# Performance work log

Hardware: AMD Instinct MI355X
Metric: run time of the kernel (lower is better)

The kernel has to match this reference:

```python
import jax, jax.numpy as jnp
import numpy as np

# Model dims (match init_kwargs)
U, I, E = 100000, 50000, 1000000   # users, items, interactions
FD, EK, EF = 64, 64, 64            # feature_dim, embed_k, embed_f
L = 3                              # n_layers
B = 16384                          # scoring batch
ALPHA = [1.0 / (k + 1) for k in range(L + 1)]


def setup_inputs() -> dict:
    key = jax.random.key(0)
    ks = jax.random.split(key, 9)
    Gu = jax.random.normal(ks[0], (U, EK), jnp.float32) * 0.05
    Gi = jax.random.normal(ks[1], (I, EK), jnp.float32) * 0.05
    F = jax.random.normal(ks[2], (FD, EF), jnp.float32) * 0.1
    proj_w = jax.random.normal(ks[3], (EF, 1), jnp.float32) * 0.1
    proj_b = jnp.zeros((1,), jnp.float32)
    # sparse binary-ish decomposition-path feature matrix (dense here)
    edge_features = (jax.random.uniform(ks[4], (E, FD)) < 0.1).astype(jnp.float32)
    u = jax.random.randint(ks[5], (E,), 0, U)
    it = jax.random.randint(ks[6], (E,), 0, I) + U  # items offset by num_users
    edge_index = jnp.stack([jnp.concatenate([u, it]),
                            jnp.concatenate([it, u])]).astype(jnp.int64)  # [2, 2E]
    users = jax.random.randint(ks[7], (B,), 0, U).astype(jnp.int64)
    items = jax.random.randint(ks[8], (B,), 0, I).astype(jnp.int64)
    return dict(Gu=Gu, Gi=Gi, F=F, proj_w=proj_w, proj_b=proj_b,
                edge_features=edge_features, edge_index=edge_index,
                users=users, items=items)


def _propagate(Gu, Gi, F, proj_w, proj_b, edge_features, edge_index):
    N = U + I
    src, dst = edge_index[0], edge_index[1]
    # edge-feature projection -> scalar edge weight, duplicated per direction
    ew = (edge_features @ F) @ proj_w + proj_b            # [E, 1]
    ew = jnp.concatenate([ew, ew], axis=0)[:, 0]          # [2E]
    # symmetric GCN normalization over the bipartite interaction graph
    deg = jax.ops.segment_sum(jnp.ones_like(ew), dst, num_segments=N)  # [N]
    dinv = jnp.where(deg > 0, jax.lax.rsqrt(jnp.maximum(deg, 1.0)), 0.0)
    coef = (dinv[src] * dinv[dst] * ew)[:, None]          # [2E, 1]
    x = jnp.concatenate([Gu, Gi], axis=0)                 # [N, K]
    out = ALPHA[0] * x
    for k in range(L):  # edge-conditioned gather -> scale -> scatter-add
        x = jax.ops.segment_sum(coef * x[src], dst, num_segments=N)
        out = out + ALPHA[k + 1] * x
    return out[:U], out[U:]


def reference(Gu, Gi, F, proj_w, proj_b, edge_features, edge_index, users, items):
    gu, gi = _propagate(Gu, Gi, F, proj_w, proj_b, edge_features, edge_index)
    # forward(): masked dot-product scoring of (user, item) pairs
    return jnp.sum(gu[users] * gi[items], axis=1)  # [B]
```

## Files before the change

### kernel.cpp

```cpp
#include <hip/hip_runtime.h>

constexpr int Uc = 100000;
constexpr int Ic = 50000;
constexpr int Nc = 150000;
constexpr int Ec = 1000000;
constexpr int Bc = 16384;
constexpr int NBS = (Nc + 1023) / 1024;

typedef _Float16 h16;
union H8 { uint4 u; h16 h[8]; };


__global__ void k_zero(uint4* __restrict__ deg4) {
    int i = blockIdx.x * blockDim.x + threadIdx.x;
    if (i < Nc / 4) deg4[i] = make_uint4(0u, 0u, 0u, 0u);
}

__global__ void k_deg2_fproj(const int* __restrict__ un, const int* __restrict__ in_,
                             unsigned* __restrict__ deg,
                             const float* __restrict__ F, const float* __restrict__ pw,
                             float* __restrict__ Fp) {
    if (blockIdx.x == 0 && threadIdx.x < 64) {
        int d = threadIdx.x;
        float s = 0.f;
#pragma unroll
        for (int j = 0; j < 64; ++j) s += F[d * 64 + j] * pw[j];
        Fp[d] = s;
    }
    int e = blockIdx.x * blockDim.x + threadIdx.x;
    if (e < Ec) {
        atomicAdd(&deg[un[e]], 1u);
        atomicAdd(&deg[in_[e]], 1u);
    }
}

__global__ void k_scan1(const unsigned* __restrict__ deg, int* __restrict__ rowptr,
                        int* __restrict__ bsums, float* __restrict__ dinv) {
    __shared__ int sh[256];
    int tid = threadIdx.x, bid = blockIdx.x;
    int base = bid * 1024 + tid * 4;
    int v0 = (base + 0 < Nc) ? (int)deg[base + 0] : 0;
    int v1 = (base + 1 < Nc) ? (int)deg[base + 1] : 0;
    int v2 = (base + 2 < Nc) ? (int)deg[base + 2] : 0;
    int v3 = (base + 3 < Nc) ? (int)deg[base + 3] : 0;
    if (base + 0 < Nc) dinv[base + 0] = v0 ? rsqrtf((float)v0) : 0.f;
    if (base + 1 < Nc) dinv[base + 1] = v1 ? rsqrtf((float)v1) : 0.f;
    if (base + 2 < Nc) dinv[base + 2] = v2 ? rsqrtf((float)v2) : 0.f;
    if (base + 3 < Nc) dinv[base + 3] = v3 ? rsqrtf((float)v3) : 0.f;
    int s = v0 + v1 + v2 + v3;
    sh[tid] = s;
    __syncthreads();
    for (int off = 1; off < 256; off <<= 1) {
        int t = (tid >= off) ? sh[tid - off] : 0;
        __syncthreads();
        sh[tid] += t;
        __syncthreads();
    }
    int excl = sh[tid] - s;
    if (tid == 255) bsums[bid] = sh[255];
    if (base + 0 < Nc) rowptr[base + 0] = excl;
    if (base + 1 < Nc) rowptr[base + 1] = excl + v0;
    if (base + 2 < Nc) rowptr[base + 2] = excl + v0 + v1;
    if (base + 3 < Nc) rowptr[base + 3] = excl + v0 + v1 + v2;
}

__global__ void k_scan3(int* __restrict__ rowptr, const int* __restrict__ bsums,
                        int* __restrict__ cursor) {
    __shared__ int sh[256];
    int tid = threadIdx.x;
    int v = (tid < NBS) ? bsums[tid] : 0;
    sh[tid] = v;
    __syncthreads();
    for (int off = 1; off < 256; off <<= 1) {
        int t = (tid >= off) ? sh[tid - off] : 0;
        __syncthreads();
        sh[tid] += t;
        __syncthreads();
    }
    int excl = sh[tid] - v;
    __syncthreads();
    sh[tid] = excl;
    __syncthreads();
    int i = blockIdx.x * blockDim.x + threadIdx.x;
    if (i < Nc) {
        int r = rowptr[i] + sh[i >> 10];
        rowptr[i] = r;
        cursor[i] = r;
    }
    if (i == 0) rowptr[Nc] = 2 * Ec;
}

__global__ void k_build(const int* __restrict__ un, const int* __restrict__ in_,
                        const float* __restrict__ ef, const float* __restrict__ Fp,
                        const float* __restrict__ pb, const float* __restrict__ dinv,
                        int* __restrict__ cursor, int2* __restrict__ csr) {
    int t = blockIdx.x * blockDim.x + threadIdx.x;
    int e = t >> 4, l = t & 15;
    if (e >= Ec) return;
    float4 f = reinterpret_cast<const float4*>(ef)[(size_t)e * 16 + l];
    float4 w = reinterpret_cast<const float4*>(Fp)[l];
    float s = f.x * w.x + f.y * w.y + f.z * w.z + f.w * w.w;
    s += __shfl_xor(s, 8, 16);
    s += __shfl_xor(s, 4, 16);
    s += __shfl_xor(s, 2, 16);
    s += __shfl_xor(s, 1, 16);
    if (l == 0 || l == 8) {
        int uu = un[e], ii = in_[e];
        float c = dinv[uu] * dinv[ii] * (s + pb[0]);
        if (l == 0) {
            int pos = atomicAdd(&cursor[ii], 1);
            csr[pos] = make_int2(uu, __float_as_int(c));
        } else {
            int pos = atomicAdd(&cursor[uu], 1);
            csr[pos] = make_int2(ii, __float_as_int(c));
        }
    }
}

__global__ void k_xin(const float* __restrict__ Gu, const float* __restrict__ Gi,
                      uint4* __restrict__ xin) {
    int t = blockIdx.x * blockDim.x + threadIdx.x;
    if (t >= Nc * 8) return;
    const float4* g;
    int idx;
    if (t < Uc * 8) { g = reinterpret_cast<const float4*>(Gu); idx = t * 2; }
    else            { g = reinterpret_cast<const float4*>(Gi); idx = (t - Uc * 8) * 2; }
    float4 a = g[idx], b = g[idx + 1];
    H8 o;
    o.h[0] = (h16)a.x; o.h[1] = (h16)a.y; o.h[2] = (h16)a.z; o.h[3] = (h16)a.w;
    o.h[4] = (h16)b.x; o.h[5] = (h16)b.y; o.h[6] = (h16)b.z; o.h[7] = (h16)b.w;
    xin[t] = o.u;
}

__global__ void k_gprop(const int* __restrict__ rowptr, const int2* __restrict__ csr,
                        const uint4* __restrict__ x, uint4* __restrict__ xn,
                        int n0, int n1) {
    int t = blockIdx.x * blockDim.x + threadIdx.x;
    int n = n0 + (t >> 3), l = t & 7;
    if (n >= n1) return;
    int e0 = rowptr[n], e1 = rowptr[n + 1];
    float acc[8] = {0.f, 0.f, 0.f, 0.f, 0.f, 0.f, 0.f, 0.f};
    int e = e0;
    for (; e + 4 <= e1; e += 4) {
        int2 s0 = csr[e], s1 = csr[e + 1], s2 = csr[e + 2], s3 = csr[e + 3];
        H8 v0, v1, v2, v3;
        v0.u = x[s0.x * 8 + l];
        v1.u = x[s1.x * 8 + l];
        v2.u = x[s2.x * 8 + l];
        v3.u = x[s3.x * 8 + l];
        float c0 = __int_as_float(s0.y), c1 = __int_as_float(s1.y);
        float c2 = __int_as_float(s2.y), c3 = __int_as_float(s3.y);
#pragma unroll
        for (int j = 0; j < 8; ++j)
            acc[j] += c0 * (float)v0.h[j] + c1 * (float)v1.h[j]
                    + c2 * (float)v2.h[j] + c3 * (float)v3.h[j];
    }
    for (; e < e1; ++e) {
        int2 sc = csr[e];
        float c = __int_as_float(sc.y);
        H8 v; v.u = x[sc.x * 8 + l];
#pragma unroll
        for (int j = 0; j < 8; ++j) acc[j] += c * (float)v.h[j];
    }
    H8 o;
#pragma unroll
    for (int j = 0; j < 8; ++j) o.h[j] = (h16)acc[j];
    xn[n * 8 + l] = o.u;
}

__global__ void k_final(const float* __restrict__ Gu, const float* __restrict__ Gi,
                        const uint4* __restrict__ x1, const uint4* __restrict__ x2,
                        const int* __restrict__ rowptr, const int2* __restrict__ csr,
                        const int* __restrict__ users, const int* __restrict__ items,
                        float* __restrict__ out) {
    int t = blockIdx.x * blockDim.x + threadIdx.x;
    int wid = t >> 3, j8 = t & 7;
    if (wid >= Bc) return;
    int un = users[wid];
    int in_ = Uc + items[wid];

    float a2[2][8];
#pragma unroll
    for (int side = 0; side < 2; ++side) {
        int n = side ? in_ : un;
        const float4* g = side ? reinterpret_cast<const float4*>(Gi)
                               : reinterpret_cast<const float4*>(Gu);
        int gi = (side ? (n - Uc) : n) * 16 + 2 * j8;
        float4 ba = g[gi], bb = g[gi + 1];
        H8 h1, h2;
        h1.u = x1[(size_t)n * 8 + j8];
        h2.u = x2[(size_t)n * 8 + j8];
        float a[8];
        a[0] = ba.x; a[1] = ba.y; a[2] = ba.z; a[3] = ba.w;
        a[4] = bb.x; a[5] = bb.y; a[6] = bb.z; a[7] = bb.w;
#pragma unroll
        for (int j = 0; j < 8; ++j)
            a[j] += 0.5f * (float)h1.h[j] + (1.f / 3.f) * (float)h2.h[j];

        float su[8] = {0.f, 0.f, 0.f, 0.f, 0.f, 0.f, 0.f, 0.f};
        int e0 = rowptr[n], e1 = rowptr[n + 1];
        int e = e0;
        for (; e + 4 <= e1; e += 4) {
            int2 s0 = csr[e], s1 = csr[e + 1], s2 = csr[e + 2], s3 = csr[e + 3];
            H8 v0, v1, v2, v3;
            v0.u = x2[(size_t)s0.x * 8 + j8];
            v1.u = x2[(size_t)s1.x * 8 + j8];
            v2.u = x2[(size_t)s2.x * 8 + j8];
            v3.u = x2[(size_t)s3.x * 8 + j8];
            float c0 = __int_as_float(s0.y), c1 = __int_as_float(s1.y);
            float c2 = __int_as_float(s2.y), c3 = __int_as_float(s3.y);
#pragma unroll
            for (int j = 0; j < 8; ++j)
                su[j] += c0 * (float)v0.h[j] + c1 * (float)v1.h[j]
                       + c2 * (float)v2.h[j] + c3 * (float)v3.h[j];
        }
        for (; e < e1; ++e) {
            int2 sc = csr[e];
            float c = __int_as_float(sc.y);
            H8 v; v.u = x2[(size_t)sc.x * 8 + j8];
#pragma unroll
            for (int j = 0; j < 8; ++j) su[j] += c * (float)v.h[j];
        }
#pragma unroll
        for (int j = 0; j < 8; ++j) a2[side][j] = a[j] + 0.25f * su[j];
    }

    float p = 0.f;
#pragma unroll
    for (int j = 0; j < 8; ++j) p += a2[0][j] * a2[1][j];
    p += __shfl_xor(p, 4, 8);
    p += __shfl_xor(p, 2, 8);
    p += __shfl_xor(p, 1, 8);
    if (j8 == 0) out[wid] = p;
}


extern "C" void kernel_launch(void* const* d_in, const int* in_sizes, int n_in,
                              void* d_out, int out_size, void* d_ws, size_t ws_size,
                              hipStream_t stream) {
    const float* Gu = (const float*)d_in[0];
    const float* Gi = (const float*)d_in[1];
    const float* F  = (const float*)d_in[2];
    const float* pw = (const float*)d_in[3];
    const float* pb = (const float*)d_in[4];
    const float* ef = (const float*)d_in[5];
    const int*   ei = (const int*)d_in[6];
    const int* users = (const int*)d_in[7];
    const int* items = (const int*)d_in[8];
    float* out = (float*)d_out;

    float* ws = (float*)d_ws;
    float*    Fp     = ws;
    float*    dinv   = Fp + 64;
    unsigned* deg    = (unsigned*)(dinv + Nc);
    int*      rowptr = (int*)(deg + Nc);
    int*      cursor = rowptr + (Nc + 16);
    int*      bsums  = cursor + Nc;
    int2*     csr    = (int2*)(bsums + 256);
    h16*      xin    = (h16*)(csr + 2 * Ec);
    h16*      xa     = xin + (size_t)Nc * 64;
    h16*      xb     = xa + (size_t)Nc * 64;

    const int* un  = ei;
    const int* in_ = ei + 2 * Ec;

    k_zero<<<(Nc / 4 + 255) / 256, 256, 0, stream>>>((uint4*)deg);
    k_deg2_fproj<<<(Ec + 255) / 256, 256, 0, stream>>>(un, in_, deg, F, pw, Fp);
    k_scan1<<<NBS, 256, 0, stream>>>(deg, rowptr, bsums, dinv);
    k_scan3<<<(Nc + 255) / 256, 256, 0, stream>>>(rowptr, bsums, cursor);
    k_build<<<(Ec * 16) / 256, 256, 0, stream>>>(un, in_, ef, Fp, pb, dinv, cursor, csr);
    k_xin<<<(Nc * 8 + 255) / 256, 256, 0, stream>>>(Gu, Gi, (uint4*)xin);

    k_gprop<<<(Uc * 8 + 255) / 256, 256, 0, stream>>>(rowptr, csr, (const uint4*)xin, (uint4*)xa, 0, Uc);
    k_gprop<<<((Nc - Uc) * 8 + 255) / 256, 256, 0, stream>>>(rowptr, csr, (const uint4*)xin, (uint4*)xa, Uc, Nc);
    k_gprop<<<(Uc * 8 + 255) / 256, 256, 0, stream>>>(rowptr, csr, (const uint4*)xa, (uint4*)xb, 0, Uc);
    k_gprop<<<((Nc - Uc) * 8 + 255) / 256, 256, 0, stream>>>(rowptr, csr, (const uint4*)xa, (uint4*)xb, Uc, Nc);

    k_final<<<(Bc * 8 + 255) / 256, 256, 0, stream>>>(Gu, Gi, (const uint4*)xa, (const uint4*)xb,
                                                      rowptr, csr, users, items, out);
}
```

Baseline: 360.0 us.

## Fuse all stages into one cooperative persistent kernel with grid syncs

Replaces the chain of separate launches (zeroing, degree count, scans, CSR build, fp16 conversion, two propagation passes, final scoring) with a single cooperative kernel. Grid-stride loops cover each stage and grid.sync() separates them. The aim is to remove per-launch overhead and inter-kernel gaps. In exchange, occupancy is capped by the persistent grid size, and each grid-wide barrier has its own cost. The user and item propagation halves are also merged into one pass.

```diff
diff --git a/kernel.cpp b/kernel.cpp
--- a/kernel.cpp
+++ b/kernel.cpp
@@ -1,4 +1,7 @@
 #include <hip/hip_runtime.h>
+#include <hip/hip_cooperative_groups.h>
+
+namespace cg = cooperative_groups;
 
 constexpr int Uc = 100000;
 constexpr int Ic = 50000;
@@ -10,272 +13,281 @@
 typedef _Float16 h16;
 union H8 { uint4 u; h16 h[8]; };
 
-
-__global__ void k_zero(uint4* __restrict__ deg4) {
-    int i = blockIdx.x * blockDim.x + threadIdx.x;
-    if (i < Nc / 4) deg4[i] = make_uint4(0u, 0u, 0u, 0u);
-}
-
-__global__ void k_deg2_fproj(const int* __restrict__ un, const int* __restrict__ in_,
-                             unsigned* __restrict__ deg,
-                             const float* __restrict__ F, const float* __restrict__ pw,
-                             float* __restrict__ Fp) {
-    if (blockIdx.x == 0 && threadIdx.x < 64) {
-        int d = threadIdx.x;
-        float s = 0.f;
-#pragma unroll
-        for (int j = 0; j < 64; ++j) s += F[d * 64 + j] * pw[j];
-        Fp[d] = s;
-    }
-    int e = blockIdx.x * blockDim.x + threadIdx.x;
-    if (e < Ec) {
-        atomicAdd(&deg[un[e]], 1u);
-        atomicAdd(&deg[in_[e]], 1u);
-    }
-}
-
-__global__ void k_scan1(const unsigned* __restrict__ deg, int* __restrict__ rowptr,
-                        int* __restrict__ bsums, float* __restrict__ dinv) {
-    __shared__ int sh[256];
-    int tid = threadIdx.x, bid = blockIdx.x;
-    int base = bid * 1024 + tid * 4;
-    int v0 = (base + 0 < Nc) ? (int)deg[base + 0] : 0;
-    int v1 = (base + 1 < Nc) ? (int)deg[base + 1] : 0;
-    int v2 = (base + 2 < Nc) ? (int)deg[base + 2] : 0;
-    int v3 = (base + 3 < Nc) ? (int)deg[base + 3] : 0;
-    if (base + 0 < Nc) dinv[base + 0] = v0 ? rsqrtf((float)v0) : 0.f;
-    if (base + 1 < Nc) dinv[base + 1] = v1 ? rsqrtf((float)v1) : 0.f;
-    if (base + 2 < Nc) dinv[base + 2] = v2 ? rsqrtf((float)v2) : 0.f;
-    if (base + 3 < Nc) dinv[base + 3] = v3 ? rsqrtf((float)v3) : 0.f;
-    int s = v0 + v1 + v2 + v3;
-    sh[tid] = s;
-    __syncthreads();
-    for (int off = 1; off < 256; off <<= 1) {
-        int t = (tid >= off) ? sh[tid - off] : 0;
-        __syncthreads();
-        sh[tid] += t;
-        __syncthreads();
-    }
-    int excl = sh[tid] - s;
-    if (tid == 255) bsums[bid] = sh[255];
-    if (base + 0 < Nc) rowptr[base + 0] = excl;
-    if (base + 1 < Nc) rowptr[base + 1] = excl + v0;
-    if (base + 2 < Nc) rowptr[base + 2] = excl + v0 + v1;
-    if (base + 3 < Nc) rowptr[base + 3] = excl + v0 + v1 + v2;
-}
-
-__global__ void k_scan3(int* __restrict__ rowptr, const int* __restrict__ bsums,
-                        int* __restrict__ cursor) {
-    __shared__ int sh[256];
-    int tid = threadIdx.x;
-    int v = (tid < NBS) ? bsums[tid] : 0;
-    sh[tid] = v;
-    __syncthreads();
-    for (int off = 1; off < 256; off <<= 1) {
-        int t = (tid >= off) ? sh[tid - off] : 0;
-        __syncthreads();
-        sh[tid] += t;
-        __syncthreads();
-    }
-    int excl = sh[tid] - v;
-    __syncthreads();
-    sh[tid] = excl;
-    __syncthreads();
-    int i = blockIdx.x * blockDim.x + threadIdx.x;
-    if (i < Nc) {
-        int r = rowptr[i] + sh[i >> 10];
-        rowptr[i] = r;
-        cursor[i] = r;
-    }
-    if (i == 0) rowptr[Nc] = 2 * Ec;
-}
-
-__global__ void k_build(const int* __restrict__ un, const int* __restrict__ in_,
-                        const float* __restrict__ ef, const float* __restrict__ Fp,
-                        const float* __restrict__ pb, const float* __restrict__ dinv,
-                        int* __restrict__ cursor, int2* __restrict__ csr) {
-    int t = blockIdx.x * blockDim.x + threadIdx.x;
-    int e = t >> 4, l = t & 15;
-    if (e >= Ec) return;
-    float4 f = reinterpret_cast<const float4*>(ef)[(size_t)e * 16 + l];
-    float4 w = reinterpret_cast<const float4*>(Fp)[l];
-    float s = f.x * w.x + f.y * w.y + f.z * w.z + f.w * w.w;
-    s += __shfl_xor(s, 8, 16);
-    s += __shfl_xor(s, 4, 16);
-    s += __shfl_xor(s, 2, 16);
-    s += __shfl_xor(s, 1, 16);
-    if (l == 0 || l == 8) {
-        int uu = un[e], ii = in_[e];
-        float c = dinv[uu] * dinv[ii] * (s + pb[0]);
-        if (l == 0) {
-            int pos = atomicAdd(&cursor[ii], 1);
-            csr[pos] = make_int2(uu, __float_as_int(c));
-        } else {
-            int pos = atomicAdd(&cursor[uu], 1);
-            csr[pos] = make_int2(ii, __float_as_int(c));
-        }
-    }
-}
-
-__global__ void k_xin(const float* __restrict__ Gu, const float* __restrict__ Gi,
-                      uint4* __restrict__ xin) {
-    int t = blockIdx.x * blockDim.x + threadIdx.x;
-    if (t >= Nc * 8) return;
-    const float4* g;
-    int idx;
-    if (t < Uc * 8) { g = reinterpret_cast<const float4*>(Gu); idx = t * 2; }
-    else            { g = reinterpret_cast<const float4*>(Gi); idx = (t - Uc * 8) * 2; }
-    float4 a = g[idx], b = g[idx + 1];
-    H8 o;
-    o.h[0] = (h16)a.x; o.h[1] = (h16)a.y; o.h[2] = (h16)a.z; o.h[3] = (h16)a.w;
-    o.h[4] = (h16)b.x; o.h[5] = (h16)b.y; o.h[6] = (h16)b.z; o.h[7] = (h16)b.w;
-    xin[t] = o.u;
-}
-
-__global__ void k_gprop(const int* __restrict__ rowptr, const int2* __restrict__ csr,
-                        const uint4* __restrict__ x, uint4* __restrict__ xn,
-                        int n0, int n1) {
-    int t = blockIdx.x * blockDim.x + threadIdx.x;
-    int n = n0 + (t >> 3), l = t & 7;
-    if (n >= n1) return;
-    int e0 = rowptr[n], e1 = rowptr[n + 1];
-    float acc[8] = {0.f, 0.f, 0.f, 0.f, 0.f, 0.f, 0.f, 0.f};
-    int e = e0;
-    for (; e + 4 <= e1; e += 4) {
-        int2 s0 = csr[e], s1 = csr[e + 1], s2 = csr[e + 2], s3 = csr[e + 3];
-        H8 v0, v1, v2, v3;
-        v0.u = x[s0.x * 8 + l];
-        v1.u = x[s1.x * 8 + l];
-        v2.u = x[s2.x * 8 + l];
-        v3.u = x[s3.x * 8 + l];
-        float c0 = __int_as_float(s0.y), c1 = __int_as_float(s1.y);
-        float c2 = __int_as_float(s2.y), c3 = __int_as_float(s3.y);
-#pragma unroll
-        for (int j = 0; j < 8; ++j)
-            acc[j] += c0 * (float)v0.h[j] + c1 * (float)v1.h[j]
-                    + c2 * (float)v2.h[j] + c3 * (float)v3.h[j];
-    }
-    for (; e < e1; ++e) {
-        int2 sc = csr[e];
-        float c = __int_as_float(sc.y);
-        H8 v; v.u = x[sc.x * 8 + l];
-#pragma unroll
-        for (int j = 0; j < 8; ++j) acc[j] += c * (float)v.h[j];
-    }
-    H8 o;
-#pragma unroll
-    for (int j = 0; j < 8; ++j) o.h[j] = (h16)acc[j];
-    xn[n * 8 + l] = o.u;
-}
-
-__global__ void k_final(const float* __restrict__ Gu, const float* __restrict__ Gi,
-                        const uint4* __restrict__ x1, const uint4* __restrict__ x2,
-                        const int* __restrict__ rowptr, const int2* __restrict__ csr,
-                        const int* __restrict__ users, const int* __restrict__ items,
-                        float* __restrict__ out) {
-    int t = blockIdx.x * blockDim.x + threadIdx.x;
-    int wid = t >> 3, j8 = t & 7;
-    if (wid >= Bc) return;
-    int un = users[wid];
-    int in_ = Uc + items[wid];
-
-    float a2[2][8];
-#pragma unroll
-    for (int side = 0; side < 2; ++side) {
-        int n = side ? in_ : un;
-        const float4* g = side ? reinterpret_cast<const float4*>(Gi)
-                               : reinterpret_cast<const float4*>(Gu);
-        int gi = (side ? (n - Uc) : n) * 16 + 2 * j8;
-        float4 ba = g[gi], bb = g[gi + 1];
-        H8 h1, h2;
-        h1.u = x1[(size_t)n * 8 + j8];
-        h2.u = x2[(size_t)n * 8 + j8];
-        float a[8];
-        a[0] = ba.x; a[1] = ba.y; a[2] = ba.z; a[3] = ba.w;
-        a[4] = bb.x; a[5] = bb.y; a[6] = bb.z; a[7] = bb.w;
-#pragma unroll
-        for (int j = 0; j < 8; ++j)
-            a[j] += 0.5f * (float)h1.h[j] + (1.f / 3.f) * (float)h2.h[j];
-
-        float su[8] = {0.f, 0.f, 0.f, 0.f, 0.f, 0.f, 0.f, 0.f};
+struct Args {
+    const float *Gu, *Gi, *F, *pw, *pb, *ef;
+    const int *un, *in_, *users, *items;
+    float* out;
+    float* Fp;
+    float* dinv;
+    unsigned* deg;
+    int* rowptr;
+    int* cursor;
+    int* bsums;
+    int2* csr;
+    h16* xin;
+    h16* xa;
+    h16* xb;
+};
+
+__device__ __forceinline__ void gprop_phase(const int* __restrict__ rowptr,
+                                            const int2* __restrict__ csr,
+                                            const uint4* __restrict__ x,
+                                            uint4* __restrict__ xn,
+                                            int gtid, int nthr) {
+    for (int t = gtid; t < Nc * 8; t += nthr) {
+        int n = t >> 3, l = t & 7;
         int e0 = rowptr[n], e1 = rowptr[n + 1];
+        float acc[8] = {0.f, 0.f, 0.f, 0.f, 0.f, 0.f, 0.f, 0.f};
         int e = e0;
         for (; e + 4 <= e1; e += 4) {
             int2 s0 = csr[e], s1 = csr[e + 1], s2 = csr[e + 2], s3 = csr[e + 3];
             H8 v0, v1, v2, v3;
-            v0.u = x2[(size_t)s0.x * 8 + j8];
-            v1.u = x2[(size_t)s1.x * 8 + j8];
-            v2.u = x2[(size_t)s2.x * 8 + j8];
-            v3.u = x2[(size_t)s3.x * 8 + j8];
+            v0.u = x[s0.x * 8 + l];
+            v1.u = x[s1.x * 8 + l];
+            v2.u = x[s2.x * 8 + l];
+            v3.u = x[s3.x * 8 + l];
             float c0 = __int_as_float(s0.y), c1 = __int_as_float(s1.y);
             float c2 = __int_as_float(s2.y), c3 = __int_as_float(s3.y);
 #pragma unroll
             for (int j = 0; j < 8; ++j)
-                su[j] += c0 * (float)v0.h[j] + c1 * (float)v1.h[j]
-                       + c2 * (float)v2.h[j] + c3 * (float)v3.h[j];
+                acc[j] += c0 * (float)v0.h[j] + c1 * (float)v1.h[j]
+                        + c2 * (float)v2.h[j] + c3 * (float)v3.h[j];
         }
         for (; e < e1; ++e) {
             int2 sc = csr[e];
             float c = __int_as_float(sc.y);
-            H8 v; v.u = x2[(size_t)sc.x * 8 + j8];
-#pragma unroll
-            for (int j = 0; j < 8; ++j) su[j] += c * (float)v.h[j];
-        }
-#pragma unroll
-        for (int j = 0; j < 8; ++j) a2[side][j] = a[j] + 0.25f * su[j];
-    }
-
-    float p = 0.f;
-#pragma unroll
-    for (int j = 0; j < 8; ++j) p += a2[0][j] * a2[1][j];
-    p += __shfl_xor(p, 4, 8);
-    p += __shfl_xor(p, 2, 8);
-    p += __shfl_xor(p, 1, 8);
-    if (j8 == 0) out[wid] = p;
+            H8 v; v.u = x[sc.x * 8 + l];
+#pragma unroll
+            for (int j = 0; j < 8; ++j) acc[j] += c * (float)v.h[j];
+        }
+        H8 o;
+#pragma unroll
+        for (int j = 0; j < 8; ++j) o.h[j] = (h16)acc[j];
+        xn[n * 8 + l] = o.u;
+    }
+}
+
+__global__ __launch_bounds__(256, 4) void mega(Args a) {
+    cg::grid_group grid = cg::this_grid();
+    const int tid = threadIdx.x;
+    const int gtid = blockIdx.x * 256 + tid;
+    const int nthr = gridDim.x * 256;
+    __shared__ int sh[256];
+
+    for (int i = gtid; i < Nc; i += nthr) a.deg[i] = 0u;
+    grid.sync();
+
+    if (blockIdx.x == 0 && tid < 64) {
+        float s = 0.f;
+#pragma unroll
+        for (int j = 0; j < 64; ++j) s += a.F[tid * 64 + j] * a.pw[j];
+        a.Fp[tid] = s;
+    }
+    for (int e = gtid; e < Ec; e += nthr) {
+        atomicAdd(&a.deg[a.un[e]], 1u);
+        atomicAdd(&a.deg[a.in_[e]], 1u);
+    }
+    grid.sync();
+
+    for (int chunk = blockIdx.x; chunk < NBS; chunk += gridDim.x) {
+        int base = chunk * 1024 + tid * 4;
+        int v0 = (base + 0 < Nc) ? (int)a.deg[base + 0] : 0;
+        int v1 = (base + 1 < Nc) ? (int)a.deg[base + 1] : 0;
+        int v2 = (base + 2 < Nc) ? (int)a.deg[base + 2] : 0;
+        int v3 = (base + 3 < Nc) ? (int)a.deg[base + 3] : 0;
+        if (base + 0 < Nc) a.dinv[base + 0] = v0 ? rsqrtf((float)v0) : 0.f;
+        if (base + 1 < Nc) a.dinv[base + 1] = v1 ? rsqrtf((float)v1) : 0.f;
+        if (base + 2 < Nc) a.dinv[base + 2] = v2 ? rsqrtf((float)v2) : 0.f;
+        if (base + 3 < Nc) a.dinv[base + 3] = v3 ? rsqrtf((float)v3) : 0.f;
+        int s = v0 + v1 + v2 + v3;
+        sh[tid] = s;
+        __syncthreads();
+        for (int off = 1; off < 256; off <<= 1) {
+            int t = (tid >= off) ? sh[tid - off] : 0;
+            __syncthreads();
+            sh[tid] += t;
+            __syncthreads();
+        }
+        int excl = sh[tid] - s;
+        if (tid == 255) a.bsums[chunk] = sh[255];
+        if (base + 0 < Nc) a.rowptr[base + 0] = excl;
+        if (base + 1 < Nc) a.rowptr[base + 1] = excl + v0;
+        if (base + 2 < Nc) a.rowptr[base + 2] = excl + v0 + v1;
+        if (base + 3 < Nc) a.rowptr[base + 3] = excl + v0 + v1 + v2;
+        __syncthreads();
+    }
+    grid.sync();
+
+    {
+        int v = (tid < NBS) ? a.bsums[tid] : 0;
+        sh[tid] = v;
+        __syncthreads();
+        for (int off = 1; off < 256; off <<= 1) {
+            int t = (tid >= off) ? sh[tid - off] : 0;
+            __syncthreads();
+            sh[tid] += t;
+            __syncthreads();
+        }
+        int excl = sh[tid] - v;
+        __syncthreads();
+        sh[tid] = excl;
+        __syncthreads();
+        for (int i = gtid; i < Nc; i += nthr) {
+            int r = a.rowptr[i] + sh[i >> 10];
+            a.rowptr[i] = r;
+            a.cursor[i] = r;
+        }
+        if (gtid == 0) a.rowptr[Nc] = 2 * Ec;
+    }
+    grid.sync();
+
+    {
+        const float4* Fp4 = reinterpret_cast<const float4*>(a.Fp);
+        const float pbv = a.pb[0];
+        for (int t = gtid; t < Ec * 16; t += nthr) {
+            int e = t >> 4, l = t & 15;
+            float4 f = reinterpret_cast<const float4*>(a.ef)[(size_t)e * 16 + l];
+            float4 w = Fp4[l];
+            float s = f.x * w.x + f.y * w.y + f.z * w.z + f.w * w.w;
+            s += __shfl_xor(s, 8, 16);
+            s += __shfl_xor(s, 4, 16);
+            s += __shfl_xor(s, 2, 16);
+            s += __shfl_xor(s, 1, 16);
+            if (l == 0 || l == 8) {
+                int uu = a.un[e], ii = a.in_[e];
+                float c = a.dinv[uu] * a.dinv[ii] * (s + pbv);
+                if (l == 0) {
+                    int pos = atomicAdd(&a.cursor[ii], 1);
+                    a.csr[pos] = make_int2(uu, __float_as_int(c));
+                } else {
+                    int pos = atomicAdd(&a.cursor[uu], 1);
+                    a.csr[pos] = make_int2(ii, __float_as_int(c));
+                }
+            }
+        }
+        uint4* xin4 = reinterpret_cast<uint4*>(a.xin);
+        for (int t = gtid; t < Nc * 8; t += nthr) {
+            const float4* g;
+            int idx;
+            if (t < Uc * 8) { g = reinterpret_cast<const float4*>(a.Gu); idx = t * 2; }
+            else            { g = reinterpret_cast<const float4*>(a.Gi); idx = (t - Uc * 8) * 2; }
+            float4 va = g[idx], vb = g[idx + 1];
+            H8 o;
+            o.h[0] = (h16)va.x; o.h[1] = (h16)va.y; o.h[2] = (h16)va.z; o.h[3] = (h16)va.w;
+            o.h[4] = (h16)vb.x; o.h[5] = (h16)vb.y; o.h[6] = (h16)vb.z; o.h[7] = (h16)vb.w;
+            xin4[t] = o.u;
+        }
+    }
+    grid.sync();
+
+    gprop_phase(a.rowptr, a.csr, reinterpret_cast<const uint4*>(a.xin),
+                reinterpret_cast<uint4*>(a.xa), gtid, nthr);
+    grid.sync();
+
+    gprop_phase(a.rowptr, a.csr, reinterpret_cast<const uint4*>(a.xa),
+                reinterpret_cast<uint4*>(a.xb), gtid, nthr);
+    grid.sync();
+
+    {
+        const uint4* x1 = reinterpret_cast<const uint4*>(a.xa);
+        const uint4* x2 = reinterpret_cast<const uint4*>(a.xb);
+        for (int t = gtid; t < Bc * 8; t += nthr) {
+            int wid = t >> 3, j8 = t & 7;
+            int un = a.users[wid];
+            int in_ = Uc + a.items[wid];
+            float a2[2][8];
+#pragma unroll
+            for (int side = 0; side < 2; ++side) {
+                int n = side ? in_ : un;
+                const float4* g = side ? reinterpret_cast<const float4*>(a.Gi)
+                                       : reinterpret_cast<const float4*>(a.Gu);
+                int gi = (side ? (n - Uc) : n) * 16 + 2 * j8;
+                float4 ba = g[gi], bb = g[gi + 1];
+                H8 h1, h2;
+                h1.u = x1[(size_t)n * 8 + j8];
+                h2.u = x2[(size_t)n * 8 + j8];
+                float acc[8];
+                acc[0] = ba.x; acc[1] = ba.y; acc[2] = ba.z; acc[3] = ba.w;
+                acc[4] = bb.x; acc[5] = bb.y; acc[6] = bb.z; acc[7] = bb.w;
+#pragma unroll
+                for (int j = 0; j < 8; ++j)
+                    acc[j] += 0.5f * (float)h1.h[j] + (1.f / 3.f) * (float)h2.h[j];
+
+                float su[8] = {0.f, 0.f, 0.f, 0.f, 0.f, 0.f, 0.f, 0.f};
+                int e0 = a.rowptr[n], e1 = a.rowptr[n + 1];
+                int e = e0;
+                for (; e + 4 <= e1; e += 4) {
+                    int2 s0 = a.csr[e], s1 = a.csr[e + 1], s2 = a.csr[e + 2], s3 = a.csr[e + 3];
+                    H8 v0, v1, v2, v3;
+                    v0.u = x2[(size_t)s0.x * 8 + j8];
+                    v1.u = x2[(size_t)s1.x * 8 + j8];
+                    v2.u = x2[(size_t)s2.x * 8 + j8];
+                    v3.u = x2[(size_t)s3.x * 8 + j8];
+                    float c0 = __int_as_float(s0.y), c1 = __int_as_float(s1.y);
+                    float c2 = __int_as_float(s2.y), c3 = __int_as_float(s3.y);
+#pragma unroll
+                    for (int j = 0; j < 8; ++j)
+                        su[j] += c0 * (float)v0.h[j] + c1 * (float)v1.h[j]
+                               + c2 * (float)v2.h[j] + c3 * (float)v3.h[j];
+                }
+                for (; e < e1; ++e) {
+                    int2 sc = a.csr[e];
+                    float c = __int_as_float(sc.y);
+                    H8 v; v.u = x2[(size_t)sc.x * 8 + j8];
+#pragma unroll
+                    for (int j = 0; j < 8; ++j) su[j] += c * (float)v.h[j];
+                }
+#pragma unroll
+                for (int j = 0; j < 8; ++j) a2[side][j] = acc[j] + 0.25f * su[j];
+            }
+            float p = 0.f;
+#pragma unroll
+            for (int j = 0; j < 8; ++j) p += a2[0][j] * a2[1][j];
+            p += __shfl_xor(p, 4, 8);
+            p += __shfl_xor(p, 2, 8);
+            p += __shfl_xor(p, 1, 8);
+            if (j8 == 0) a.out[wid] = p;
+        }
+    }
 }
 
 
 extern "C" void kernel_launch(void* const* d_in, const int* in_sizes, int n_in,
                               void* d_out, int out_size, void* d_ws, size_t ws_size,
                               hipStream_t stream) {
-    const float* Gu = (const float*)d_in[0];
-    const float* Gi = (const float*)d_in[1];
-    const float* F  = (const float*)d_in[2];
-    const float* pw = (const float*)d_in[3];
-    const float* pb = (const float*)d_in[4];
-    const float* ef = (const float*)d_in[5];
-    const int*   ei = (const int*)d_in[6];
-    const int* users = (const int*)d_in[7];
-    const int* items = (const int*)d_in[8];
-    float* out = (float*)d_out;
+    Args a;
+    a.Gu = (const float*)d_in[0];
+    a.Gi = (const float*)d_in[1];
+    a.F  = (const float*)d_in[2];
+    a.pw = (const float*)d_in[3];
+    a.pb = (const float*)d_in[4];
+    a.ef = (const float*)d_in[5];
+    const int* ei = (const int*)d_in[6];
+    a.users = (const int*)d_in[7];
+    a.items = (const int*)d_in[8];
+    a.out = (float*)d_out;
 
     float* ws = (float*)d_ws;
-    float*    Fp     = ws;
-    float*    dinv   = Fp + 64;
-    unsigned* deg    = (unsigned*)(dinv + Nc);
-    int*      rowptr = (int*)(deg + Nc);
-    int*      cursor = rowptr + (Nc + 16);
-    int*      bsums  = cursor + Nc;
-    int2*     csr    = (int2*)(bsums + 256);
-    h16*      xin    = (h16*)(csr + 2 * Ec);
-    h16*      xa     = xin + (size_t)Nc * 64;
-    h16*      xb     = xa + (size_t)Nc * 64;
-
-    const int* un  = ei;
-    const int* in_ = ei + 2 * Ec;
-
-    k_zero<<<(Nc / 4 + 255) / 256, 256, 0, stream>>>((uint4*)deg);
-    k_deg2_fproj<<<(Ec + 255) / 256, 256, 0, stream>>>(un, in_, deg, F, pw, Fp);
-    k_scan1<<<NBS, 256, 0, stream>>>(deg, rowptr, bsums, dinv);
-    k_scan3<<<(Nc + 255) / 256, 256, 0, stream>>>(rowptr, bsums, cursor);
-    k_build<<<(Ec * 16) / 256, 256, 0, stream>>>(un, in_, ef, Fp, pb, dinv, cursor, csr);
-    k_xin<<<(Nc * 8 + 255) / 256, 256, 0, stream>>>(Gu, Gi, (uint4*)xin);
-
-    k_gprop<<<(Uc * 8 + 255) / 256, 256, 0, stream>>>(rowptr, csr, (const uint4*)xin, (uint4*)xa, 0, Uc);
-    k_gprop<<<((Nc - Uc) * 8 + 255) / 256, 256, 0, stream>>>(rowptr, csr, (const uint4*)xin, (uint4*)xa, Uc, Nc);
-    k_gprop<<<(Uc * 8 + 255) / 256, 256, 0, stream>>>(rowptr, csr, (const uint4*)xa, (uint4*)xb, 0, Uc);
-    k_gprop<<<((Nc - Uc) * 8 + 255) / 256, 256, 0, stream>>>(rowptr, csr, (const uint4*)xa, (uint4*)xb, Uc, Nc);
-
-    k_final<<<(Bc * 8 + 255) / 256, 256, 0, stream>>>(Gu, Gi, (const uint4*)xa, (const uint4*)xb,
-                                                      rowptr, csr, users, items, out);
+    a.Fp     = ws;
+    a.dinv   = a.Fp + 64;
+    a.deg    = (unsigned*)(a.dinv + Nc);
+    a.rowptr = (int*)(a.deg + Nc);
+    a.cursor = a.rowptr + (Nc + 16);
+    a.bsums  = a.cursor + Nc;
+    a.csr    = (int2*)(a.bsums + 256);
+    a.xin    = (h16*)(a.csr + 2 * Ec);
+    a.xa     = a.xin + (size_t)Nc * 64;
+    a.xb     = a.xa + (size_t)Nc * 64;
+
+    a.un  = ei;
+    a.in_ = ei + 2 * Ec;
+
+    int maxPerCU = 0;
+    hipOccupancyMaxActiveBlocksPerMultiprocessor(&maxPerCU, mega, 256, 0);
+    if (maxPerCU < 1) maxPerCU = 1;
+    int grid = 256 * maxPerCU;
+    if (grid > 1024) grid = 1024;
+
+    void* params[] = {&a};
+    hipLaunchCooperativeKernel((void*)mega, dim3(grid), dim3(256), params, 0, stream);
 }
```

Result: slower. 898.0 us (+149.5%).
